# Optimization experiments

Measured on AMD Instinct MI355X. Metric: run time of the kernel, lower is better.

The kernel has to match this reference:

```python
import jax, jax.numpy as jnp
import numpy as np

D_MODEL = 1024
NUM_HEADS = 16
HEAD_DIM = D_MODEL // NUM_HEADS


def setup_inputs() -> dict:
    key = jax.random.key(0)
    ks = jax.random.split(key, 5)
    x = jax.random.normal(ks[0], (4, 2048, D_MODEL), dtype=jnp.float32)
    # xavier_uniform with gain=0.1 for square (D,D) weights: limit = 0.1*sqrt(6/(D+D))
    limit = 0.1 * np.sqrt(6.0 / (2 * D_MODEL))
    def w(k):
        return jax.random.uniform(k, (D_MODEL, D_MODEL), jnp.float32, -limit, limit)
    return {
        "x": x,
        "W_q": w(ks[1]), "b_q": jnp.zeros((D_MODEL,), jnp.float32),
        "W_k": w(ks[2]), "b_k": jnp.zeros((D_MODEL,), jnp.float32),
        "W_v": w(ks[3]), "b_v": jnp.zeros((D_MODEL,), jnp.float32),
        "W_o": w(ks[4]), "b_o": jnp.zeros((D_MODEL,), jnp.float32),
    }


def reference(x, W_q, b_q, W_k, b_k, W_v, b_v, W_o, b_o):
    B, S, D = x.shape
    H, Hd = NUM_HEADS, HEAD_DIM
    # Linear: x @ W^T + b (torch nn.Linear convention); weights here are (out, in)
    def proj(W, b):
        y = jnp.einsum('bsd,ed->bse', x, W) + b
        return y.reshape(B, S, H, Hd).transpose(0, 2, 1, 3)  # [B,H,S,Hd]
    Q = proj(W_q, b_q)
    K = proj(W_k, b_k)
    V = proj(W_v, b_v)
    scale = 1.0 / np.sqrt(Hd).astype(np.float32)
    scores = jnp.einsum('bhqd,bhkd->bhqk', Q, K) * scale  # [B,H,S,S]
    attn = jax.nn.softmax(scores, axis=-1)
    ctx = jnp.einsum('bhqk,bhkd->bhqd', attn, V)
    ctx = ctx.transpose(0, 2, 1, 3).reshape(B, S, D)
    out = jnp.einsum('bsd,ed->bse', ctx, W_o) + b_o
    return out
```

## Files before the change

kernel.cpp:

```cpp
#include <hip/hip_runtime.h>
#include <math.h>

#define B_  4
#define S_  2048
#define D_  1024
#define H_  16
#define HD_ 64
#define M_  (B_*S_)

typedef short short8 __attribute__((ext_vector_type(8)));
typedef float f32x4 __attribute__((ext_vector_type(4)));

#define MFMA16(a,b,c) __builtin_amdgcn_mfma_f32_16x16x32_bf16(a, b, c, 0, 0, 0)

#if __has_builtin(__builtin_amdgcn_exp2f)
#define EXP2(x) __builtin_amdgcn_exp2f(x)
#else
#define EXP2(x) exp2f(x)
#endif

__device__ __forceinline__ unsigned short f2bf(float f) {
    unsigned u = __float_as_uint(f);
    u = (u + 0x7FFF + ((u >> 16) & 1)) >> 16;
    return (unsigned short)u;
}

__device__ __forceinline__ unsigned pack_bf16(float a, float b) {
#if __has_builtin(__builtin_amdgcn_cvt_pk_bf16_f32)
    typedef __bf16 bf2 __attribute__((ext_vector_type(2)));
    bf2 v = __builtin_amdgcn_cvt_pk_bf16_f32(a, b);
    unsigned r;
    __builtin_memcpy(&r, &v, 4);
    return r;
#else
    unsigned ua = __float_as_uint(a), ub = __float_as_uint(b);
    ua += 0x7FFFu + ((ua >> 16) & 1u);
    ub += 0x7FFFu + ((ub >> 16) & 1u);
    return __builtin_amdgcn_perm(ub, ua, 0x07060302u);
#endif
}

__device__ __forceinline__ void async_copy16(const void* g, void* l) {
    __builtin_amdgcn_global_load_lds(
        (const __attribute__((address_space(1))) void*)g,
        (__attribute__((address_space(3))) void*)l, 16, 0, 0);
}

__global__ __launch_bounds__(256) void cvt_all(
    const float* __restrict__ x,
    const float* __restrict__ w0, const float* __restrict__ w1,
    const float* __restrict__ w2, const float* __restrict__ w3,
    unsigned short* __restrict__ xb, unsigned short* __restrict__ wb)
{
    size_t i = ((size_t)blockIdx.x * 256 + threadIdx.x) * 4;
    const float* src; unsigned short* dst;
    if (i < (size_t)M_ * D_) {
        src = x + i; dst = xb + i;
    } else {
        size_t j = i - (size_t)M_ * D_;
        int z = (int)(j >> 20);
        const float* w = (z == 0) ? w0 : (z == 1) ? w1 : (z == 2) ? w2 : w3;
        src = w + (j & ((size_t)D_ * D_ - 1)); dst = wb + j;
    }
    float4 v = *(const float4*)src;
    uint2 o;
    o.x = pack_bf16(v.x, v.y);
    o.y = pack_bf16(v.z, v.w);
    *(uint2*)dst = o;
}

__device__ __forceinline__ void gemm_body(
    const unsigned short* __restrict__ A, const unsigned short* __restrict__ W,
    const float* __restrict__ bias, void* __restrict__ out,
    int mode, float cscale, int bx, int by)
{
    __shared__ unsigned short As[128 * 64];
    __shared__ unsigned short Ws[128 * 64];
    const int K = D_;
    int tid = threadIdx.x;
    int w = tid >> 6, lane = tid & 63;
    int quad = lane >> 4, l16 = lane & 15;
    int r8 = lane >> 3, c8 = lane & 7;
    int cK = c8 ^ r8;
    int wm = w >> 2, wn = w & 3;
    int m0 = by * 128, n0 = bx * 128;
    int fl = l16 & 7;

    f32x4 acc[4][2];
    #pragma unroll
    for (int i = 0; i < 4; ++i)
        #pragma unroll
        for (int j = 0; j < 2; ++j)
            acc[i][j] = (f32x4){0.f, 0.f, 0.f, 0.f};

    const unsigned short* Ag = A + (size_t)(m0 + w * 8 + r8) * K + cK * 8;
    const unsigned short* Wg = W + (size_t)(n0 + w * 8 + r8) * K + cK * 8;

    for (int k0 = 0; k0 < K; k0 += 64) {
        __syncthreads();
        #pragma unroll
        for (int ii = 0; ii < 2; ++ii) {
            async_copy16(Ag + k0 + (size_t)ii * 64 * K, As + (ii * 64 + w * 8) * 64);
            async_copy16(Wg + k0 + (size_t)ii * 64 * K, Ws + (ii * 64 + w * 8) * 64);
        }
        __syncthreads();
        #pragma unroll
        for (int s = 0; s < 2; ++s) {
            int st = ((quad + s * 4) ^ fl) * 8;
            short8 a[4], b[2];
            #pragma unroll
            for (int i = 0; i < 4; ++i)
                a[i] = *(const short8*)&As[(wm * 64 + i * 16 + l16) * 64 + st];
            #pragma unroll
            for (int j = 0; j < 2; ++j)
                b[j] = *(const short8*)&Ws[(wn * 32 + j * 16 + l16) * 64 + st];
            #pragma unroll
            for (int i = 0; i < 4; ++i)
                #pragma unroll
                for (int j = 0; j < 2; ++j)
                    acc[i][j] = MFMA16(a[i], b[j], acc[i][j]);
        }
    }

    #pragma unroll
    for (int i = 0; i < 4; ++i) {
        int mb = m0 + wm * 64 + i * 16 + quad * 4;
        #pragma unroll
        for (int j = 0; j < 2; ++j) {
            int n = n0 + wn * 32 + j * 16 + l16;
            float bn = bias[n];
            if (mode == 0) {
                #pragma unroll
                for (int r = 0; r < 4; ++r)
                    ((float*)out)[(size_t)(mb + r) * D_ + n] = acc[i][j][r] + bn;
            } else if (mode == 1) {
                int h = n >> 6, hd = n & 63;
                #pragma unroll
                for (int r = 0; r < 4; ++r) {
                    int m = mb + r;
                    int bb = m >> 11, s = m & (S_ - 1);
                    ((unsigned short*)out)[(((size_t)(bb * H_ + h)) * S_ + s) * HD_ + hd] =
                        f2bf((acc[i][j][r] + bn) * cscale);
                }
            } else {
                int h = n >> 6, hd = n & 63;
                int bb = mb >> 11, s0 = mb & (S_ - 1);
                uint2 o;
                o.x = pack_bf16(acc[i][j][0] + bn, acc[i][j][1] + bn);
                o.y = pack_bf16(acc[i][j][2] + bn, acc[i][j][3] + bn);
                *(uint2*)&((unsigned short*)out)[(((size_t)(bb * H_ + h)) * HD_ + hd) * S_ + s0] = o;
            }
        }
    }
}

__global__ __launch_bounds__(512) void qkv_gemm(
    const unsigned short* __restrict__ A,
    const unsigned short* __restrict__ Wq, const unsigned short* __restrict__ Wk,
    const unsigned short* __restrict__ Wv,
    const float* __restrict__ bq, const float* __restrict__ bk, const float* __restrict__ bv,
    unsigned short* Qo, unsigned short* Ko, unsigned short* Vo)
{
    int z = blockIdx.z;
    const unsigned short* W = (z == 0) ? Wq : (z == 1) ? Wk : Wv;
    const float* bias = (z == 0) ? bq : (z == 1) ? bk : bv;
    unsigned short* out = (z == 0) ? Qo : (z == 1) ? Ko : Vo;
    float cscale = (z == 0) ? 0.125f * 1.44269504088896f : 1.0f;
    int mode = (z == 2) ? 2 : 1;
    gemm_body(A, W, bias, out, mode, cscale, blockIdx.x, blockIdx.y);
}

__global__ __launch_bounds__(512) void out_gemm(
    const unsigned short* __restrict__ A, const unsigned short* __restrict__ W,
    const float* __restrict__ bias, float* __restrict__ out)
{
    gemm_body(A, W, bias, out, 0, 1.0f, blockIdx.x, blockIdx.y);
}

__global__ __launch_bounds__(256) void attn_mfma(
    const unsigned short* __restrict__ Q, const unsigned short* __restrict__ K,
    const unsigned short* __restrict__ VT, unsigned short* __restrict__ ctx)
{
    __shared__ unsigned short Ks[64 * 64];
    __shared__ unsigned short VTs[64 * 64];
    __shared__ unsigned short QPs[128 * 64];

    int tid = threadIdx.x;
    int w = tid >> 6, lane = tid & 63;
    int quad = lane >> 4, l16 = lane & 15;
    int r8 = lane >> 3, c8 = lane & 7;
    int cK = c8 ^ r8;
    int fl  = l16 & 7;
    int fl2 = (l16 ^ (l16 >> 1)) & 7;
    int bh = blockIdx.y;
    int q0 = blockIdx.x * 128;

    const unsigned short* Qp = Q + ((size_t)bh * S_ + q0) * HD_;
    const unsigned short* Kp = K + (size_t)bh * S_ * HD_;
    const unsigned short* Vp = VT + (size_t)bh * HD_ * S_;

    #pragma unroll
    for (int ii = 0; ii < 4; ++ii) {
        int cQ = c8 ^ r8 ^ (r8 >> 1) ^ ((ii & 1) * 4);
        async_copy16(Qp + (size_t)(w * 32 + ii * 8 + r8) * HD_ + cQ * 8,
                     QPs + (w * 32 + ii * 8) * 64);
    }
    __syncthreads();

    short8 bq_[2][2];
    #pragma unroll
    for (int mt = 0; mt < 2; ++mt)
        #pragma unroll
        for (int s = 0; s < 2; ++s)
            bq_[mt][s] = *(const short8*)&QPs[(w * 32 + mt * 16 + l16) * 64 +
                                              (((quad + s * 4) ^ fl2) * 8)];

    f32x4 O[2][4];
    float lsum[2] = {0.f, 0.f};
    #pragma unroll
    for (int mt = 0; mt < 2; ++mt)
        #pragma unroll
        for (int nt = 0; nt < 4; ++nt) O[mt][nt] = (f32x4){0.f, 0.f, 0.f, 0.f};

    for (int kt = 0; kt < S_ / 64; ++kt) {
        __syncthreads();
        #pragma unroll
        for (int ih = 0; ih < 2; ++ih) {
            int rb = w * 16 + ih * 8;
            async_copy16(Kp + (size_t)(kt * 64 + rb + r8) * HD_ + cK * 8, Ks + rb * 64);
            async_copy16(Vp + (size_t)(rb + r8) * S_ + kt * 64 + cK * 8, VTs + rb * 64);
        }
        __syncthreads();

        f32x4 sc[2][4];
        #pragma unroll
        for (int mt = 0; mt < 2; ++mt)
            #pragma unroll
            for (int nt = 0; nt < 4; ++nt) sc[mt][nt] = (f32x4){0.f, 0.f, 0.f, 0.f};
        #pragma unroll
        for (int s = 0; s < 2; ++s) {
            int stk = ((quad + s * 4) ^ fl) * 8;
            #pragma unroll
            for (int nt = 0; nt < 4; ++nt) {
                short8 ak = *(const short8*)&Ks[(nt * 16 + l16) * 64 + stk];
                sc[0][nt] = MFMA16(ak, bq_[0][s], sc[0][nt]);
                sc[1][nt] = MFMA16(ak, bq_[1][s], sc[1][nt]);
            }
        }

        #pragma unroll
        for (int mt = 0; mt < 2; ++mt) {
            #pragma unroll
            for (int nt = 0; nt < 4; ++nt) {
                float p0 = EXP2(sc[mt][nt][0]);
                float p1 = EXP2(sc[mt][nt][1]);
                float p2 = EXP2(sc[mt][nt][2]);
                float p3 = EXP2(sc[mt][nt][3]);
                lsum[mt] += (p0 + p1) + (p2 + p3);
                ushort4 pk;
                pk.x = f2bf(p0); pk.y = f2bf(p1); pk.z = f2bf(p2); pk.w = f2bf(p3);
                int addr = (w * 32 + mt * 16 + l16) * 64 +
                           (((nt * 2 + (quad >> 1)) ^ fl2) * 8) + (quad & 1) * 4;
                *(ushort4*)&QPs[addr] = pk;
            }
        }

        #pragma unroll
        for (int s = 0; s < 2; ++s) {
            int stp = ((quad + s * 4) ^ fl2) * 8;
            int stv = ((quad + s * 4) ^ fl) * 8;
            short8 pa0 = *(const short8*)&QPs[(w * 32 + l16) * 64 + stp];
            short8 pa1 = *(const short8*)&QPs[(w * 32 + 16 + l16) * 64 + stp];
            #pragma unroll
            for (int nt = 0; nt < 4; ++nt) {
                short8 bv_ = *(const short8*)&VTs[(nt * 16 + l16) * 64 + stv];
                O[0][nt] = MFMA16(pa0, bv_, O[0][nt]);
                O[1][nt] = MFMA16(pa1, bv_, O[1][nt]);
            }
        }
    }

    float linv[2];
    #pragma unroll
    for (int mt = 0; mt < 2; ++mt) {
        float l = lsum[mt];
        l += __shfl_xor(l, 16);
        l += __shfl_xor(l, 32);
        linv[mt] = 1.0f / l;
    }

    int b = bh >> 4, h = bh & (H_ - 1);
    #pragma unroll
    for (int mt = 0; mt < 2; ++mt)
        #pragma unroll
        for (int r = 0; r < 4; ++r) {
            float inv = __shfl(linv[mt], quad * 4 + r, 64);
            int q = q0 + w * 32 + mt * 16 + quad * 4 + r;
            size_t base = ((size_t)(b * S_) + q) * D_ + h * HD_;
            #pragma unroll
            for (int nt = 0; nt < 4; ++nt)
                ctx[base + nt * 16 + l16] = f2bf(O[mt][nt][r] * inv);
        }
}

extern "C" void kernel_launch(void* const* d_in, const int* in_sizes, int n_in,
                              void* d_out, int out_size, void* d_ws, size_t ws_size,
                              hipStream_t stream) {
    const float* x  = (const float*)d_in[0];
    const float* Wq = (const float*)d_in[1];
    const float* bq = (const float*)d_in[2];
    const float* Wk = (const float*)d_in[3];
    const float* bk = (const float*)d_in[4];
    const float* Wv = (const float*)d_in[5];
    const float* bv = (const float*)d_in[6];
    const float* Wo = (const float*)d_in[7];
    const float* bo = (const float*)d_in[8];

    unsigned short* xb  = (unsigned short*)d_ws;
    unsigned short* wb  = xb + (size_t)M_ * D_;
    unsigned short* Qb  = wb + (size_t)4 * D_ * D_;
    unsigned short* Kb  = Qb + (size_t)M_ * D_;
    unsigned short* VTb = Kb + (size_t)M_ * D_;
    unsigned short* ctb = VTb + (size_t)M_ * D_;

    int cvt_blocks = (M_ * D_ + 4 * D_ * D_) / 1024;
    cvt_all<<<cvt_blocks, 256, 0, stream>>>(x, Wq, Wk, Wv, Wo, xb, wb);

    qkv_gemm<<<dim3(D_ / 128, M_ / 128, 3), 512, 0, stream>>>(
        xb, wb, wb + (size_t)D_ * D_, wb + (size_t)2 * D_ * D_,
        bq, bk, bv, Qb, Kb, VTb);

    attn_mfma<<<dim3(S_ / 128, B_ * H_), 256, 0, stream>>>(Qb, Kb, VTb, ctb);

    out_gemm<<<dim3(D_ / 128, M_ / 128), 512, 0, stream>>>(
        ctb, wb + (size_t)3 * D_ * D_, bo, (float*)d_out);
}
```

Before: 309.2 us.

## Double-buffer K/V tiles in attention with 512-thread blocks over 256 queries

```diff
diff --git a/kernel.cpp b/kernel.cpp
--- a/kernel.cpp
+++ b/kernel.cpp
@@ -177,13 +177,13 @@
     gemm_body(A, W, bias, out, 0, 1.0f, blockIdx.x, blockIdx.y);
 }
 
-__global__ __launch_bounds__(256) void attn_mfma(
+__global__ __launch_bounds__(512, 4) void attn_mfma(
     const unsigned short* __restrict__ Q, const unsigned short* __restrict__ K,
     const unsigned short* __restrict__ VT, unsigned short* __restrict__ ctx)
 {
-    __shared__ unsigned short Ks[64 * 64];
-    __shared__ unsigned short VTs[64 * 64];
-    __shared__ unsigned short QPs[128 * 64];
+    __shared__ unsigned short Ks[2 * 64 * 64];
+    __shared__ unsigned short VTs[2 * 64 * 64];
+    __shared__ unsigned short QPs[256 * 64];
 
     int tid = threadIdx.x;
     int w = tid >> 6, lane = tid & 63;
@@ -192,19 +192,20 @@
     int cK = c8 ^ r8;
     int fl  = l16 & 7;
     int fl2 = (l16 ^ (l16 >> 1)) & 7;
-    int bh = blockIdx.y;
-    int q0 = blockIdx.x * 128;
+    int bh = blockIdx.x;
+    int q0 = blockIdx.y * 256;
 
     const unsigned short* Qp = Q + ((size_t)bh * S_ + q0) * HD_;
     const unsigned short* Kp = K + (size_t)bh * S_ * HD_;
     const unsigned short* Vp = VT + (size_t)bh * HD_ * S_;
 
-    #pragma unroll
-    for (int ii = 0; ii < 4; ++ii) {
-        int cQ = c8 ^ r8 ^ (r8 >> 1) ^ ((ii & 1) * 4);
-        async_copy16(Qp + (size_t)(w * 32 + ii * 8 + r8) * HD_ + cQ * 8,
-                     QPs + (w * 32 + ii * 8) * 64);
-    }
+    int cQ = c8 ^ r8 ^ (r8 >> 1) ^ ((w & 1) * 4);
+    #pragma unroll
+    for (int ii = 0; ii < 4; ++ii)
+        async_copy16(Qp + (size_t)(ii * 64 + w * 8 + r8) * HD_ + cQ * 8,
+                     QPs + (ii * 64 + w * 8) * 64);
+    async_copy16(Kp + (size_t)(w * 8 + r8) * HD_ + cK * 8, Ks + (w * 8) * 64);
+    async_copy16(Vp + (size_t)(w * 8 + r8) * S_ + cK * 8, VTs + (w * 8) * 64);
     __syncthreads();
 
     short8 bq_[2][2];
@@ -222,15 +223,17 @@
         #pragma unroll
         for (int nt = 0; nt < 4; ++nt) O[mt][nt] = (f32x4){0.f, 0.f, 0.f, 0.f};
 
+    int cur = 0;
     for (int kt = 0; kt < S_ / 64; ++kt) {
-        __syncthreads();
-        #pragma unroll
-        for (int ih = 0; ih < 2; ++ih) {
-            int rb = w * 16 + ih * 8;
-            async_copy16(Kp + (size_t)(kt * 64 + rb + r8) * HD_ + cK * 8, Ks + rb * 64);
-            async_copy16(Vp + (size_t)(rb + r8) * S_ + kt * 64 + cK * 8, VTs + rb * 64);
-        }
-        __syncthreads();
+        if (kt + 1 < S_ / 64) {
+            int nb = (cur ^ 1) * 4096;
+            async_copy16(Kp + (size_t)((kt + 1) * 64 + w * 8 + r8) * HD_ + cK * 8,
+                         Ks + nb + (w * 8) * 64);
+            async_copy16(Vp + (size_t)(w * 8 + r8) * S_ + (kt + 1) * 64 + cK * 8,
+                         VTs + nb + (w * 8) * 64);
+        }
+        const unsigned short* ks  = Ks + cur * 4096;
+        const unsigned short* vts = VTs + cur * 4096;
 
         f32x4 sc[2][4];
         #pragma unroll
@@ -242,7 +245,7 @@
             int stk = ((quad + s * 4) ^ fl) * 8;
             #pragma unroll
             for (int nt = 0; nt < 4; ++nt) {
-                short8 ak = *(const short8*)&Ks[(nt * 16 + l16) * 64 + stk];
+                short8 ak = *(const short8*)&ks[(nt * 16 + l16) * 64 + stk];
                 sc[0][nt] = MFMA16(ak, bq_[0][s], sc[0][nt]);
                 sc[1][nt] = MFMA16(ak, bq_[1][s], sc[1][nt]);
             }
@@ -257,11 +260,12 @@
                 float p2 = EXP2(sc[mt][nt][2]);
                 float p3 = EXP2(sc[mt][nt][3]);
                 lsum[mt] += (p0 + p1) + (p2 + p3);
-                ushort4 pk;
-                pk.x = f2bf(p0); pk.y = f2bf(p1); pk.z = f2bf(p2); pk.w = f2bf(p3);
+                uint2 pk;
+                pk.x = pack_bf16(p0, p1);
+                pk.y = pack_bf16(p2, p3);
                 int addr = (w * 32 + mt * 16 + l16) * 64 +
                            (((nt * 2 + (quad >> 1)) ^ fl2) * 8) + (quad & 1) * 4;
-                *(ushort4*)&QPs[addr] = pk;
+                *(uint2*)&QPs[addr] = pk;
             }
         }
 
@@ -273,11 +277,14 @@
             short8 pa1 = *(const short8*)&QPs[(w * 32 + 16 + l16) * 64 + stp];
             #pragma unroll
             for (int nt = 0; nt < 4; ++nt) {
-                short8 bv_ = *(const short8*)&VTs[(nt * 16 + l16) * 64 + stv];
+                short8 bv_ = *(const short8*)&vts[(nt * 16 + l16) * 64 + stv];
                 O[0][nt] = MFMA16(pa0, bv_, O[0][nt]);
                 O[1][nt] = MFMA16(pa1, bv_, O[1][nt]);
             }
         }
+
+        __syncthreads();
+        cur ^= 1;
     }
 
     float linv[2];
@@ -330,7 +337,7 @@
         xb, wb, wb + (size_t)D_ * D_, wb + (size_t)2 * D_ * D_,
         bq, bk, bv, Qb, Kb, VTb);
 
-    attn_mfma<<<dim3(S_ / 128, B_ * H_), 256, 0, stream>>>(Qb, Kb, VTb, ctb);
+    attn_mfma<<<dim3(B_ * H_, S_ / 256), 512, 0, stream>>>(Qb, Kb, VTb, ctb);
 
     out_gemm<<<dim3(D_ / 128, M_ / 128), 512, 0, stream>>>(
         ctb, wb + (size_t)3 * D_ * D_, bo, (float*)d_out);
```

Measured after the change: 286.8 us. 1.08x faster.
